# Kernel tuning notes

Measured on AMD Instinct MI355X. Metric: run time of the kernel, lower is better.

The kernel has to match this reference:

```python
import jax, jax.numpy as jnp
import numpy as np

B, S, D = 2, 2048, 2048
H, HD = 16, 128          # num_heads, head_dim (H*HD == D)
I = 4096                 # intermediate_size; ffn in-dim is 2*I
EPS = 1e-5


def rmsnorm(x, w):
    return x * jax.lax.rsqrt(jnp.mean(x * x, axis=-1, keepdims=True) + EPS) * w


def setup_inputs() -> dict:
    key = jax.random.key(0)
    ks = jax.random.split(key, 12)
    sd = 0.02
    return {
        "hidden_states": jax.random.normal(ks[0], (B, S, D), jnp.float32),
        "attention_mask": jnp.zeros((B, S), jnp.float32),  # additive mask
        "rn1_w": jnp.ones((D,), jnp.float32),
        "wq": jax.random.normal(ks[1], (D, D), jnp.float32) * sd,
        "wk": jax.random.normal(ks[2], (D, D), jnp.float32) * sd,
        "wv": jax.random.normal(ks[3], (D, D), jnp.float32) * sd,
        "wo": jax.random.normal(ks[4], (D, D), jnp.float32) * sd,
        "rn2_w": jnp.ones((D,), jnp.float32),
        "w1": jax.random.normal(ks[5], (D, 2 * I), jnp.float32) * sd,      # Linear(d, 2*I, bias=False)
        "fc1_w": jax.random.normal(ks[6], (2 * I, I), jnp.float32) * sd,   # SwiGLU fc1
        "fc1_b": jnp.zeros((I,), jnp.float32),
        "fc2_w": jax.random.normal(ks[7], (2 * I, I), jnp.float32) * sd,   # SwiGLU fc2
        "fc2_b": jnp.zeros((I,), jnp.float32),
        "w3": jax.random.normal(ks[8], (I, D), jnp.float32) * sd,          # Linear(I, d, bias=False)
    }


def reference(hidden_states, attention_mask, rn1_w, wq, wk, wv, wo, rn2_w,
              w1, fc1_w, fc1_b, fc2_w, fc2_b, w3):
    # --- attention ---
    attn_in = rmsnorm(hidden_states, rn1_w)
    q = (attn_in @ wq).reshape(B, S, H, HD)
    k = (attn_in @ wk).reshape(B, S, H, HD)
    v = (attn_in @ wv).reshape(B, S, H, HD)
    # rope_cache is None -> no rotary embedding applied
    scores = jnp.einsum("bqhd,bkhd->bhqk", q, k) / np.sqrt(HD).astype(np.float32)
    scores = scores + attention_mask[:, None, None, :]  # [B,1,1,S] broadcast
    probs = jax.nn.softmax(scores, axis=-1)             # dropout p=0 (eval)
    attn = jnp.einsum("bhqk,bkhd->bqhd", probs, v).reshape(B, S, D)
    residual1 = hidden_states + attn @ wo
    # --- SwiGLU FFN ---
    ffn_in = rmsnorm(residual1, rn2_w)
    x = ffn_in @ w1                                      # [B,S,2I]
    gated = jax.nn.silu(x @ fc1_w + fc1_b) * (x @ fc2_w + fc2_b)  # [B,S,I]
    return residual1 + gated @ w3
```

## Files before the change

### kernel.cpp

```cpp
#include <hip/hip_runtime.h>
#include <hip/hip_bf16.h>
#include <stdint.h>

using short8 = __attribute__((ext_vector_type(8))) short;
using f32x4  = __attribute__((ext_vector_type(4))) float;

#define DEV __device__ __forceinline__

DEV float b2f(unsigned short u) {
  union { unsigned int i; float f; } v; v.i = ((unsigned int)u) << 16; return v.f;
}
DEV unsigned short f2b(float f) {
  union { float f; unsigned int i; } v; v.f = f;
  unsigned int x = v.i;
  return (unsigned short)((x + 0x7FFFu + ((x >> 16) & 1u)) >> 16);
}
DEV void g2lds16(const void* g, void* l) {
  __builtin_amdgcn_global_load_lds((const __attribute__((address_space(1))) void*)g,
                                   (__attribute__((address_space(3))) void*)l, 16, 0, 0);
}

enum { EPI_BF16 = 0, EPI_RESID_F32 = 1, EPI_BIAS_BF16 = 2, EPI_RESID_OUT = 3 };

template<int EPI>
__global__ __launch_bounds__(512, 2)
void gemm_bt256(const unsigned short* __restrict__ A, const unsigned short* __restrict__ Bt,
                void* __restrict__ Cout, const void* __restrict__ extra,
                int M, int N, int K) {
  __shared__ __align__(16) unsigned short As[2][256 * 64];
  __shared__ __align__(16) unsigned short Bs[2][256 * 64];
  const int nbx = N >> 8;
  int wg = blockIdx.x;
  const int nwg = gridDim.x;
  if ((nwg & 7) == 0) wg = (wg & 7) * (nwg >> 3) + (wg >> 3);
  const int by = wg / nbx, bx = wg % nbx;
  const int m0 = by << 8, n0 = bx << 8;
  const int t = threadIdx.x;
  const int l = t & 63, wid = t >> 6;
  const int lr = l & 15, lg = l >> 4;
  const int wr = (wid >> 2) << 7;
  const int wc = (wid & 3) << 6;

  f32x4 acc[8][4];
#pragma unroll
  for (int i = 0; i < 8; ++i)
#pragma unroll
    for (int j = 0; j < 4; ++j) acc[i][j] = (f32x4){0.f, 0.f, 0.f, 0.f};

  const int sr = t >> 3;
  const int scSwz = ((t & 7) << 3) ^ ((sr & 7) << 3);
  const unsigned short* Ag = A  + (size_t)(m0 + sr) * K + scSwz;
  const unsigned short* Bg = Bt + (size_t)(n0 + sr) * K + scSwz;

  const int xorv = (lr & 7) << 3;
  const int cb0 = (lg * 8) ^ xorv;
  const int cb1 = (32 + lg * 8) ^ xorv;

#pragma unroll
  for (int ld = 0; ld < 4; ++ld) {
    g2lds16(Ag + (size_t)(ld * 64) * K, &As[0][0] + t * 8 + ld * 4096);
    g2lds16(Bg + (size_t)(ld * 64) * K, &Bs[0][0] + t * 8 + ld * 4096);
  }
  asm volatile("s_waitcnt vmcnt(0)\n\ts_barrier" ::: "memory");

  int cur = 0;
  for (int kt = 0; kt < K; kt += 64) {
    const unsigned short* Asc = &As[0][0] + cur * 16384;
    const unsigned short* Bsc = &Bs[0][0] + cur * 16384;
    unsigned short* Asn = &As[0][0] + (cur ^ 1) * 16384;
    unsigned short* Bsn = &Bs[0][0] + (cur ^ 1) * 16384;
    const bool has_next = (kt + 64) < K;
    short8 bfr[4][2];
#pragma unroll
    for (int p = 0; p < 4; ++p) {
      short8 af[2][2];
#pragma unroll
      for (int a = 0; a < 2; ++a) {
        const int ro = (wr + (p * 2 + a) * 16 + lr) << 6;
        af[a][0] = *(const short8*)(Asc + ro + cb0);
        af[a][1] = *(const short8*)(Asc + ro + cb1);
      }
      if (p == 0) {
#pragma unroll
        for (int ni = 0; ni < 4; ++ni) {
          const int ro = (wc + ni * 16 + lr) << 6;
          bfr[ni][0] = *(const short8*)(Bsc + ro + cb0);
          bfr[ni][1] = *(const short8*)(Bsc + ro + cb1);
        }
        if (has_next) {
#pragma unroll
          for (int ld = 0; ld < 4; ++ld)
            g2lds16(Ag + (size_t)(ld * 64) * K + (kt + 64), Asn + t * 8 + ld * 4096);
        }
      }
      if (p == 1 && has_next) {
#pragma unroll
        for (int ld = 0; ld < 4; ++ld)
          g2lds16(Bg + (size_t)(ld * 64) * K + (kt + 64), Bsn + t * 8 + ld * 4096);
      }
      asm volatile("s_barrier" ::: "memory");
      asm volatile("s_waitcnt lgkmcnt(0)" ::: "memory");
      __builtin_amdgcn_sched_barrier(0);
      __builtin_amdgcn_s_setprio(1);
#pragma unroll
      for (int kk = 0; kk < 2; ++kk)
#pragma unroll
        for (int a = 0; a < 2; ++a)
#pragma unroll
          for (int ni = 0; ni < 4; ++ni)
            acc[p * 2 + a][ni] =
                __builtin_amdgcn_mfma_f32_16x16x32_bf16(af[a][kk], bfr[ni][kk], acc[p * 2 + a][ni], 0, 0, 0);
      __builtin_amdgcn_s_setprio(0);
      if (p < 3) {
        asm volatile("s_barrier" ::: "memory");
      } else {
        asm volatile("s_waitcnt vmcnt(0)\n\ts_barrier" ::: "memory");
      }
    }
    cur ^= 1;
  }

#pragma unroll
  for (int mi = 0; mi < 8; ++mi) {
#pragma unroll
    for (int ni = 0; ni < 4; ++ni) {
      const int col = n0 + wc + ni * 16 + lr;
#pragma unroll
      for (int j = 0; j < 4; ++j) {
        const int row = m0 + wr + mi * 16 + lg * 4 + j;
        const size_t idx = (size_t)row * N + col;
        const float v = acc[mi][ni][j];
        if constexpr (EPI == EPI_BF16) {
          ((unsigned short*)Cout)[idx] = f2b(v);
        } else if constexpr (EPI == EPI_RESID_F32) {
          ((float*)Cout)[idx] = v + ((const float*)extra)[idx];
        } else if constexpr (EPI == EPI_BIAS_BF16) {
          ((unsigned short*)Cout)[idx] = f2b(v + ((const float*)extra)[col]);
        } else {
          ((float*)Cout)[idx] = v + ((const float*)extra)[idx];
        }
      }
    }
  }
}

template<int EPI>
__global__ __launch_bounds__(256)
void gemm_bt(const unsigned short* __restrict__ A, const unsigned short* __restrict__ Bt,
             void* __restrict__ Cout, const void* __restrict__ extra,
             int M, int N, int K) {
  __shared__ __align__(16) unsigned short As[128 * 64];
  __shared__ __align__(16) unsigned short Bs[128 * 64];
  const int nbx = N >> 7;
  int wg = blockIdx.x;
  const int nwg = gridDim.x;
  if ((nwg & 7) == 0) wg = (wg & 7) * (nwg >> 3) + (wg >> 3);
  const int by = wg / nbx, bx = wg % nbx;
  const int m0 = by << 7, n0 = bx << 7;
  const int t = threadIdx.x;
  const int l = t & 63, w = t >> 6;
  const int lr = l & 15, lg = l >> 4;
  const int wr = (w >> 1) << 6, wc = (w & 1) << 6;

  f32x4 acc[4][4];
#pragma unroll
  for (int i = 0; i < 4; ++i)
#pragma unroll
    for (int j = 0; j < 4; ++j) acc[i][j] = (f32x4){0.f, 0.f, 0.f, 0.f};

  const int sr = t >> 3;
  const int skSwz = ((t & 7) << 3) ^ ((sr & 7) << 3);
  const unsigned short* Ag = A  + (size_t)(m0 + sr) * K + skSwz;
  const unsigned short* Bg = Bt + (size_t)(n0 + sr) * K + skSwz;
  unsigned short* Al = As + t * 8;
  unsigned short* Bl = Bs + t * 8;

  for (int kt = 0; kt < K; kt += 64) {
#pragma unroll
    for (int c = 0; c < 4; ++c) {
      g2lds16(Ag + (size_t)(c * 32) * K + kt, Al + c * 2048);
      g2lds16(Bg + (size_t)(c * 32) * K + kt, Bl + c * 2048);
    }
    __syncthreads();
#pragma unroll
    for (int ks = 0; ks < 2; ++ks) {
      short8 af[4], bfr[4];
#pragma unroll
      for (int mi = 0; mi < 4; ++mi) {
        const int row = wr + mi * 16 + lr;
        af[mi] = *(const short8*)(As + (row << 6) + (((ks * 32 + lg * 8)) ^ ((row & 7) << 3)));
      }
#pragma unroll
      for (int ni = 0; ni < 4; ++ni) {
        const int row = wc + ni * 16 + lr;
        bfr[ni] = *(const short8*)(Bs + (row << 6) + (((ks * 32 + lg * 8)) ^ ((row & 7) << 3)));
      }
#pragma unroll
      for (int mi = 0; mi < 4; ++mi)
#pragma unroll
        for (int ni = 0; ni < 4; ++ni)
          acc[mi][ni] = __builtin_amdgcn_mfma_f32_16x16x32_bf16(af[mi], bfr[ni], acc[mi][ni], 0, 0, 0);
    }
    __syncthreads();
  }

#pragma unroll
  for (int mi = 0; mi < 4; ++mi) {
#pragma unroll
    for (int ni = 0; ni < 4; ++ni) {
      const int col = n0 + wc + ni * 16 + lr;
#pragma unroll
      for (int j = 0; j < 4; ++j) {
        const int row = m0 + wr + mi * 16 + lg * 4 + j;
        const size_t idx = (size_t)row * N + col;
        const float v = acc[mi][ni][j];
        if constexpr (EPI == EPI_BF16) {
          ((unsigned short*)Cout)[idx] = f2b(v);
        } else if constexpr (EPI == EPI_RESID_F32) {
          ((float*)Cout)[idx] = v + ((const float*)extra)[idx];
        } else if constexpr (EPI == EPI_BIAS_BF16) {
          ((unsigned short*)Cout)[idx] = f2b(v + ((const float*)extra)[col]);
        } else {
          ((float*)Cout)[idx] = v + ((const float*)extra)[idx];
        }
      }
    }
  }
}

__global__ __launch_bounds__(256)
void attn_fwd(const unsigned short* __restrict__ qkv, const unsigned short* __restrict__ vt,
              const float* __restrict__ mask, unsigned short* __restrict__ out) {
  __shared__ __align__(16) unsigned short Ks[64 * 128];
  __shared__ __align__(16) unsigned short Vs[128 * 64];
  __shared__ __align__(16) unsigned short Ps[4][16 * 64];
  const int b = blockIdx.z, hh = blockIdx.y;
  const int q0 = blockIdx.x << 6;
  const int t = threadIdx.x, l = t & 63, w = t >> 6;
  const int lr = l & 15, lg = l >> 4;
  const float scale = 0.08838834764831845f;

  short8 qf[4];
  {
    const unsigned short* qb = qkv + (size_t)(b * 2048 + q0 + w * 16 + lr) * 6144 + hh * 128;
#pragma unroll
    for (int ks = 0; ks < 4; ++ks) qf[ks] = *(const short8*)(qb + ks * 32 + lg * 8);
  }
  f32x4 acc_o[8];
#pragma unroll
  for (int i = 0; i < 8; ++i) acc_o[i] = (f32x4){0.f, 0.f, 0.f, 0.f};
  float m_r[4], l_r[4];
#pragma unroll
  for (int j = 0; j < 4; ++j) { m_r[j] = -1e30f; l_r[j] = 0.f; }

  const unsigned short* kb = qkv + (size_t)(b * 2048) * 6144 + 2048 + hh * 128;
  const unsigned short* vb = vt + (size_t)(b * 16 + hh) * 128 * 2048;
  const float* mb = mask + b * 2048;

  for (int kt = 0; kt < 2048; kt += 64) {
#pragma unroll
    for (int c = 0; c < 4; ++c) {
      const int e = (c * 256 + t) * 8;
      const int kr = e >> 7, kc = e & 127;
      g2lds16(kb + (size_t)(kt + kr) * 6144 + (kc ^ ((kr & 7) << 3)), Ks + e);
      const int vr = e >> 6, vc = e & 63;
      g2lds16(vb + (size_t)vr * 2048 + kt + (vc ^ ((vr & 7) << 3)), Vs + e);
    }
    __syncthreads();

    f32x4 sc[4];
#pragma unroll
    for (int nt = 0; nt < 4; ++nt) {
      f32x4 s = (f32x4){0.f, 0.f, 0.f, 0.f};
#pragma unroll
      for (int ks = 0; ks < 4; ++ks) {
        short8 kf = *(const short8*)(Ks + ((nt * 16 + lr) << 7) + ((ks * 32 + lg * 8) ^ ((lr & 7) << 3)));
        s = __builtin_amdgcn_mfma_f32_16x16x32_bf16(qf[ks], kf, s, 0, 0, 0);
      }
      sc[nt] = s;
    }
#pragma unroll
    for (int nt = 0; nt < 4; ++nt) {
      const float mv = mb[kt + nt * 16 + lr];
#pragma unroll
      for (int j = 0; j < 4; ++j) sc[nt][j] = sc[nt][j] * scale + mv;
    }
#pragma unroll
    for (int j = 0; j < 4; ++j) {
      float tm = fmaxf(fmaxf(sc[0][j], sc[1][j]), fmaxf(sc[2][j], sc[3][j]));
      tm = fmaxf(tm, __shfl_xor(tm, 1));
      tm = fmaxf(tm, __shfl_xor(tm, 2));
      tm = fmaxf(tm, __shfl_xor(tm, 4));
      tm = fmaxf(tm, __shfl_xor(tm, 8));
      const float mn = fmaxf(m_r[j], tm);
      const float corr = __expf(m_r[j] - mn);
      m_r[j] = mn;
      float ps = 0.f;
#pragma unroll
      for (int nt = 0; nt < 4; ++nt) {
        const float p = __expf(sc[nt][j] - mn);
        sc[nt][j] = p;
        ps += p;
      }
      ps += __shfl_xor(ps, 1);
      ps += __shfl_xor(ps, 2);
      ps += __shfl_xor(ps, 4);
      ps += __shfl_xor(ps, 8);
      l_r[j] = l_r[j] * corr + ps;
#pragma unroll
      for (int di = 0; di < 8; ++di) acc_o[di][j] *= corr;
    }
#pragma unroll
    for (int nt = 0; nt < 4; ++nt)
#pragma unroll
      for (int j = 0; j < 4; ++j) {
        const int q = lg * 4 + j;
        Ps[w][(q << 6) + ((nt * 16 + lr) ^ ((q & 7) << 3))] = f2b(sc[nt][j]);
      }
    asm volatile("s_waitcnt lgkmcnt(0)" ::: "memory");
#pragma unroll
    for (int ks2 = 0; ks2 < 2; ++ks2) {
      short8 pf = *(const short8*)(&Ps[w][(lr << 6) + ((ks2 * 32 + lg * 8) ^ ((lr & 7) << 3))]);
#pragma unroll
      for (int di = 0; di < 8; ++di) {
        short8 vf = *(const short8*)(Vs + ((di * 16 + lr) << 6) + ((ks2 * 32 + lg * 8) ^ ((lr & 7) << 3)));
        acc_o[di] = __builtin_amdgcn_mfma_f32_16x16x32_bf16(pf, vf, acc_o[di], 0, 0, 0);
      }
    }
    __syncthreads();
  }
#pragma unroll
  for (int di = 0; di < 8; ++di)
#pragma unroll
    for (int j = 0; j < 4; ++j) {
      const int q = q0 + w * 16 + lg * 4 + j;
      out[(size_t)(b * 2048 + q) * 2048 + hh * 128 + di * 16 + lr] = f2b(acc_o[di][j] / l_r[j]);
    }
}

__global__ __launch_bounds__(256)
void rmsnorm_k(const float* __restrict__ in, const float* __restrict__ wgt,
               unsigned short* __restrict__ out) {
  __shared__ float red[4];
  const int row = blockIdx.x, t = threadIdx.x;
  const float4* rp = (const float4*)(in + (size_t)row * 2048 + t * 8);
  float4 a = rp[0], b = rp[1];
  float x[8] = {a.x, a.y, a.z, a.w, b.x, b.y, b.z, b.w};
  float s = 0.f;
#pragma unroll
  for (int i = 0; i < 8; ++i) s += x[i] * x[i];
#pragma unroll
  for (int m = 1; m < 64; m <<= 1) s += __shfl_xor(s, m);
  const int l = t & 63, w = t >> 6;
  if (l == 0) red[w] = s;
  __syncthreads();
  const float tot = red[0] + red[1] + red[2] + red[3];
  const float rr = rsqrtf(tot * (1.f / 2048.f) + 1e-5f);
  const float4* wp = (const float4*)(wgt + t * 8);
  float4 wa = wp[0], wb = wp[1];
  float ww[8] = {wa.x, wa.y, wa.z, wa.w, wb.x, wb.y, wb.z, wb.w};
  short8 o;
#pragma unroll
  for (int i = 0; i < 8; ++i) o[i] = (short)f2b(x[i] * rr * ww[i]);
  *(short8*)(out + (size_t)row * 2048 + t * 8) = o;
}

__global__ __launch_bounds__(256)
void transpose2d(const float* __restrict__ in, unsigned short* __restrict__ out,
                 int R, int C) {
  __shared__ __align__(16) unsigned short tile[64][72];
  const int r0 = blockIdx.y << 6, c0 = blockIdx.x << 6;
  const int t = threadIdx.x;
#pragma unroll
  for (int it = 0; it < 4; ++it) {
    const int e = (it * 256 + t) * 4;
    const int r = e >> 6, cc = e & 63;
    float4 v = *(const float4*)(in + (size_t)(r0 + r) * C + c0 + cc);
    tile[cc + 0][r] = f2b(v.x);
    tile[cc + 1][r] = f2b(v.y);
    tile[cc + 2][r] = f2b(v.z);
    tile[cc + 3][r] = f2b(v.w);
  }
  __syncthreads();
#pragma unroll
  for (int it = 0; it < 2; ++it) {
    const int e = (it * 256 + t) * 8;
    const int rr = e >> 6, kk = e & 63;
    short8 v = *(const short8*)(&tile[rr][kk]);
    *(short8*)(out + (size_t)(c0 + rr) * R + r0 + kk) = v;
  }
}

__global__ __launch_bounds__(256)
void transpose_v(const unsigned short* __restrict__ qkv, unsigned short* __restrict__ vt) {
  __shared__ __align__(16) unsigned short tile[64][72];
  const int s0 = blockIdx.x << 6, d0 = blockIdx.y << 6;
  const int z = blockIdx.z;
  const unsigned short* in = qkv + (size_t)((z >> 4) * 2048) * 6144 + 4096 + (z & 15) * 128;
  unsigned short* outp = vt + (size_t)z * 128 * 2048;
  const int t = threadIdx.x;
#pragma unroll
  for (int it = 0; it < 2; ++it) {
    const int e = (it * 256 + t) * 8;
    const int r = e >> 6, cc = e & 63;
    short8 v = *(const short8*)(in + (size_t)(s0 + r) * 6144 + d0 + cc);
#pragma unroll
    for (int i = 0; i < 8; ++i) tile[cc + i][r] = (unsigned short)v[i];
  }
  __syncthreads();
#pragma unroll
  for (int it = 0; it < 2; ++it) {
    const int e = (it * 256 + t) * 8;
    const int rr = e >> 6, kk = e & 63;
    short8 v = *(const short8*)(&tile[rr][kk]);
    *(short8*)(outp + (size_t)(d0 + rr) * 2048 + s0 + kk) = v;
  }
}

__global__ __launch_bounds__(256)
void swiglu_k(const unsigned short* __restrict__ g1, const unsigned short* __restrict__ g2,
              unsigned short* __restrict__ gated) {
  const size_t i = ((size_t)blockIdx.x * 256 + threadIdx.x) * 8;
  short8 a = *(const short8*)(g1 + i);
  short8 b = *(const short8*)(g2 + i);
  short8 o;
#pragma unroll
  for (int j = 0; j < 8; ++j) {
    const float x = b2f((unsigned short)a[j]);
    const float y = b2f((unsigned short)b[j]);
    o[j] = (short)f2b(x / (1.f + __expf(-x)) * y);
  }
  *(short8*)(gated + i) = o;
}

extern "C" void kernel_launch(void* const* d_in, const int* in_sizes, int n_in,
                              void* d_out, int out_size, void* d_ws, size_t ws_size,
                              hipStream_t stream) {
  const float* h    = (const float*)d_in[0];
  const float* mask = (const float*)d_in[1];
  const float* rn1w = (const float*)d_in[2];
  const float* wq   = (const float*)d_in[3];
  const float* wk   = (const float*)d_in[4];
  const float* wv   = (const float*)d_in[5];
  const float* wo   = (const float*)d_in[6];
  const float* rn2w = (const float*)d_in[7];
  const float* w1   = (const float*)d_in[8];
  const float* fc1w = (const float*)d_in[9];
  const float* fc1b = (const float*)d_in[10];
  const float* fc2w = (const float*)d_in[11];
  const float* fc2b = (const float*)d_in[12];
  const float* w3   = (const float*)d_in[13];

  char* ws = (char*)d_ws;
  size_t off = 0;
  auto alloc = [&](size_t bytes) { char* p = ws + off; off += (bytes + 255) & ~(size_t)255; return p; };
  unsigned short* bufA = (unsigned short*)alloc(16777216);
  unsigned short* bufB = (unsigned short*)alloc(16777216);
  unsigned short* qkv  = (unsigned short*)alloc(50331648);
  float*          r1f  = (float*)alloc(33554432);
  unsigned short* xbuf = (unsigned short*)alloc(67108864);
  unsigned short* g1   = (unsigned short*)alloc(33554432);
  unsigned short* g2   = (unsigned short*)alloc(33554432);
  unsigned short* wt   = (unsigned short*)alloc(67108864);
  if (off > ws_size) return;

  rmsnorm_k<<<4096, 256, 0, stream>>>(h, rn1w, bufA);
  transpose2d<<<dim3(32, 32), 256, 0, stream>>>(wq, wt,                 2048, 2048);
  transpose2d<<<dim3(32, 32), 256, 0, stream>>>(wk, wt + 2048 * 2048,   2048, 2048);
  transpose2d<<<dim3(32, 32), 256, 0, stream>>>(wv, wt + 2 * 2048 * 2048, 2048, 2048);
  gemm_bt256<EPI_BF16><<<384, 512, 0, stream>>>(bufA, wt, qkv, nullptr, 4096, 6144, 2048);
  transpose_v<<<dim3(32, 2, 32), 256, 0, stream>>>(qkv, bufB);
  attn_fwd<<<dim3(32, 16, 2), 256, 0, stream>>>(qkv, bufB, mask, bufA);
  transpose2d<<<dim3(32, 32), 256, 0, stream>>>(wo, wt, 2048, 2048);
  gemm_bt<EPI_RESID_F32><<<512, 256, 0, stream>>>(bufA, wt, r1f, h, 4096, 2048, 2048);

  rmsnorm_k<<<4096, 256, 0, stream>>>(r1f, rn2w, bufB);
  transpose2d<<<dim3(128, 32), 256, 0, stream>>>(w1, wt, 2048, 8192);
  gemm_bt256<EPI_BF16><<<512, 512, 0, stream>>>(bufB, wt, xbuf, nullptr, 4096, 8192, 2048);
  transpose2d<<<dim3(64, 128), 256, 0, stream>>>(fc1w, wt, 8192, 4096);
  gemm_bt256<EPI_BIAS_BF16><<<256, 512, 0, stream>>>(xbuf, wt, g1, fc1b, 4096, 4096, 8192);
  transpose2d<<<dim3(64, 128), 256, 0, stream>>>(fc2w, wt, 8192, 4096);
  gemm_bt256<EPI_BIAS_BF16><<<256, 512, 0, stream>>>(xbuf, wt, g2, fc2b, 4096, 4096, 8192);
  unsigned short* gated = qkv;
  swiglu_k<<<8192, 256, 0, stream>>>(g1, g2, gated);
  transpose2d<<<dim3(32, 64), 256, 0, stream>>>(w3, wt, 4096, 2048);
  gemm_bt<EPI_RESID_OUT><<<512, 256, 0, stream>>>(gated, wt, d_out, r1f, 4096, 2048, 4096);
}
```

Before: 1.225 ms.

## Prefetch B tiles two K-steps ahead using register-held fragments in GEMM pipeline

The GEMM main loop now issues the B-operand global-to-LDS loads two K tiles ahead instead of one, while A stays one tile ahead. This is safe because B fragments for the current tile are already pulled into registers at the first sub-step. Waits are relaxed from vmcnt(0) to vmcnt(4), so the next B tile's loads can stay in flight across the tile boundary. The aim is to hide more global-load latency behind the MFMA work. The cost is that correctness now depends on careful wait-count accounting and barrier ordering.

```diff
diff --git a/kernel.cpp b/kernel.cpp
--- a/kernel.cpp
+++ b/kernel.cpp
@@ -51,25 +51,38 @@
   const int scSwz = ((t & 7) << 3) ^ ((sr & 7) << 3);
   const unsigned short* Ag = A  + (size_t)(m0 + sr) * K + scSwz;
   const unsigned short* Bg = Bt + (size_t)(n0 + sr) * K + scSwz;
+  const int nT = K >> 6;
+
+  auto stageA = [&](int tt, int h) {
+    unsigned short* dst = &As[tt & 1][h * 8192 + t * 8];
+    const unsigned short* src = Ag + (size_t)(h * 128) * K + (tt << 6);
+    g2lds16(src, dst);
+    g2lds16(src + (size_t)64 * K, dst + 4096);
+  };
+  auto stageB = [&](int tt, int h) {
+    unsigned short* dst = &Bs[tt & 1][h * 8192 + t * 8];
+    const unsigned short* src = Bg + (size_t)(h * 128) * K + (tt << 6);
+    g2lds16(src, dst);
+    g2lds16(src + (size_t)64 * K, dst + 4096);
+  };
 
   const int xorv = (lr & 7) << 3;
   const int cb0 = (lg * 8) ^ xorv;
   const int cb1 = (32 + lg * 8) ^ xorv;
 
-#pragma unroll
-  for (int ld = 0; ld < 4; ++ld) {
-    g2lds16(Ag + (size_t)(ld * 64) * K, &As[0][0] + t * 8 + ld * 4096);
-    g2lds16(Bg + (size_t)(ld * 64) * K, &Bs[0][0] + t * 8 + ld * 4096);
-  }
-  asm volatile("s_waitcnt vmcnt(0)\n\ts_barrier" ::: "memory");
-
-  int cur = 0;
-  for (int kt = 0; kt < K; kt += 64) {
-    const unsigned short* Asc = &As[0][0] + cur * 16384;
-    const unsigned short* Bsc = &Bs[0][0] + cur * 16384;
-    unsigned short* Asn = &As[0][0] + (cur ^ 1) * 16384;
-    unsigned short* Bsn = &Bs[0][0] + (cur ^ 1) * 16384;
-    const bool has_next = (kt + 64) < K;
+  stageA(0, 0); stageA(0, 1); stageB(0, 0); stageB(0, 1);
+  if (nT > 1) {
+    stageB(1, 0); stageB(1, 1);
+    asm volatile("s_waitcnt vmcnt(4)" ::: "memory");
+  } else {
+    asm volatile("s_waitcnt vmcnt(0)" ::: "memory");
+  }
+  asm volatile("s_barrier" ::: "memory");
+
+  for (int tt = 0; tt < nT; ++tt) {
+    const int cur = tt & 1;
+    const unsigned short* Asc = &As[cur][0];
+    const unsigned short* Bsc = &Bs[cur][0];
     short8 bfr[4][2];
 #pragma unroll
     for (int p = 0; p < 4; ++p) {
@@ -87,17 +100,11 @@
           bfr[ni][0] = *(const short8*)(Bsc + ro + cb0);
           bfr[ni][1] = *(const short8*)(Bsc + ro + cb1);
         }
-        if (has_next) {
-#pragma unroll
-          for (int ld = 0; ld < 4; ++ld)
-            g2lds16(Ag + (size_t)(ld * 64) * K + (kt + 64), Asn + t * 8 + ld * 4096);
-        }
-      }
-      if (p == 1 && has_next) {
-#pragma unroll
-        for (int ld = 0; ld < 4; ++ld)
-          g2lds16(Bg + (size_t)(ld * 64) * K + (kt + 64), Bsn + t * 8 + ld * 4096);
-      }
+        if (tt + 1 < nT) stageA(tt + 1, 0);
+      }
+      if (p == 1 && tt + 1 < nT) stageA(tt + 1, 1);
+      if (p == 2 && tt + 2 < nT) stageB(tt + 2, 0);
+      if (p == 3 && tt + 2 < nT) stageB(tt + 2, 1);
       asm volatile("s_barrier" ::: "memory");
       asm volatile("s_waitcnt lgkmcnt(0)" ::: "memory");
       __builtin_amdgcn_sched_barrier(0);
@@ -114,10 +121,13 @@
       if (p < 3) {
         asm volatile("s_barrier" ::: "memory");
       } else {
-        asm volatile("s_waitcnt vmcnt(0)\n\ts_barrier" ::: "memory");
-      }
-    }
-    cur ^= 1;
+        if (tt + 1 < nT) {
+          if (tt + 2 < nT) asm volatile("s_waitcnt vmcnt(4)" ::: "memory");
+          else             asm volatile("s_waitcnt vmcnt(0)" ::: "memory");
+        }
+        asm volatile("s_barrier" ::: "memory");
+      }
+    }
   }
 
 #pragma unroll
```

New measurement: 1.267 ms. 1.03x slower.

## Software-pipeline LDS fragment reads with double-buffered A registers in GEMM main loop

Applied to the files above, without the earlier changes.

Restructures the GEMM K-loop so A-fragment LDS reads for the next phase are issued before the MFMAs of the current phase, ping-ponging between two register sets. The next tile's A and B fragments are prefetched at the end of each iteration, and partial lgkmcnt waits replace the full waits. The goal is to hide LDS read latency behind MFMA work and drop some barriers. It uses more VGPRs, which may lower occupancy, and the partial waitcnt counts must match the issued loads exactly.

```diff
diff --git a/kernel.cpp b/kernel.cpp
--- a/kernel.cpp
+++ b/kernel.cpp
@@ -51,74 +51,108 @@
   const int scSwz = ((t & 7) << 3) ^ ((sr & 7) << 3);
   const unsigned short* Ag = A  + (size_t)(m0 + sr) * K + scSwz;
   const unsigned short* Bg = Bt + (size_t)(n0 + sr) * K + scSwz;
+  const int nT = K >> 6;
+
+  auto stageA = [&](int tt) {
+    unsigned short* dst = &As[tt & 1][t * 8];
+    const unsigned short* src = Ag + ((size_t)tt << 6);
+#pragma unroll
+    for (int ld = 0; ld < 4; ++ld) g2lds16(src + (size_t)(ld * 64) * K, dst + ld * 4096);
+  };
+  auto stageB = [&](int tt) {
+    unsigned short* dst = &Bs[tt & 1][t * 8];
+    const unsigned short* src = Bg + ((size_t)tt << 6);
+#pragma unroll
+    for (int ld = 0; ld < 4; ++ld) g2lds16(src + (size_t)(ld * 64) * K, dst + ld * 4096);
+  };
 
   const int xorv = (lr & 7) << 3;
   const int cb0 = (lg * 8) ^ xorv;
   const int cb1 = (32 + lg * 8) ^ xorv;
 
-#pragma unroll
-  for (int ld = 0; ld < 4; ++ld) {
-    g2lds16(Ag + (size_t)(ld * 64) * K, &As[0][0] + t * 8 + ld * 4096);
-    g2lds16(Bg + (size_t)(ld * 64) * K, &Bs[0][0] + t * 8 + ld * 4096);
-  }
+  short8 afA[2][2], afB[2][2], bfr[4][2];
+
+#define READ_A(dst, base, p)                                          \
+  {                                                                   \
+    const int ro0 = (wr + ((p) * 2 + 0) * 16 + lr) << 6;              \
+    const int ro1 = (wr + ((p) * 2 + 1) * 16 + lr) << 6;              \
+    dst[0][0] = *(const short8*)((base) + ro0 + cb0);                 \
+    dst[0][1] = *(const short8*)((base) + ro0 + cb1);                 \
+    dst[1][0] = *(const short8*)((base) + ro1 + cb0);                 \
+    dst[1][1] = *(const short8*)((base) + ro1 + cb1);                 \
+  }
+#define READ_B(base)                                                  \
+  {                                                                   \
+    _Pragma("unroll")                                                 \
+    for (int ni = 0; ni < 4; ++ni) {                                  \
+      const int ro = (wc + ni * 16 + lr) << 6;                        \
+      bfr[ni][0] = *(const short8*)((base) + ro + cb0);               \
+      bfr[ni][1] = *(const short8*)((base) + ro + cb1);               \
+    }                                                                 \
+  }
+#define MFMA_PH(af, r0)                                               \
+  {                                                                   \
+    _Pragma("unroll")                                                 \
+    for (int kk = 0; kk < 2; ++kk)                                    \
+      _Pragma("unroll")                                               \
+      for (int a = 0; a < 2; ++a)                                     \
+        _Pragma("unroll")                                             \
+        for (int ni = 0; ni < 4; ++ni)                                \
+          acc[(r0) + a][ni] = __builtin_amdgcn_mfma_f32_16x16x32_bf16(\
+              af[a][kk], bfr[ni][kk], acc[(r0) + a][ni], 0, 0, 0);    \
+  }
+
+  stageA(0); stageB(0);
   asm volatile("s_waitcnt vmcnt(0)\n\ts_barrier" ::: "memory");
-
-  int cur = 0;
-  for (int kt = 0; kt < K; kt += 64) {
-    const unsigned short* Asc = &As[0][0] + cur * 16384;
-    const unsigned short* Bsc = &Bs[0][0] + cur * 16384;
-    unsigned short* Asn = &As[0][0] + (cur ^ 1) * 16384;
-    unsigned short* Bsn = &Bs[0][0] + (cur ^ 1) * 16384;
-    const bool has_next = (kt + 64) < K;
-    short8 bfr[4][2];
-#pragma unroll
-    for (int p = 0; p < 4; ++p) {
-      short8 af[2][2];
-#pragma unroll
-      for (int a = 0; a < 2; ++a) {
-        const int ro = (wr + (p * 2 + a) * 16 + lr) << 6;
-        af[a][0] = *(const short8*)(Asc + ro + cb0);
-        af[a][1] = *(const short8*)(Asc + ro + cb1);
-      }
-      if (p == 0) {
-#pragma unroll
-        for (int ni = 0; ni < 4; ++ni) {
-          const int ro = (wc + ni * 16 + lr) << 6;
-          bfr[ni][0] = *(const short8*)(Bsc + ro + cb0);
-          bfr[ni][1] = *(const short8*)(Bsc + ro + cb1);
-        }
-        if (has_next) {
-#pragma unroll
-          for (int ld = 0; ld < 4; ++ld)
-            g2lds16(Ag + (size_t)(ld * 64) * K + (kt + 64), Asn + t * 8 + ld * 4096);
-        }
-      }
-      if (p == 1 && has_next) {
-#pragma unroll
-        for (int ld = 0; ld < 4; ++ld)
-          g2lds16(Bg + (size_t)(ld * 64) * K + (kt + 64), Bsn + t * 8 + ld * 4096);
-      }
-      asm volatile("s_barrier" ::: "memory");
-      asm volatile("s_waitcnt lgkmcnt(0)" ::: "memory");
-      __builtin_amdgcn_sched_barrier(0);
-      __builtin_amdgcn_s_setprio(1);
-#pragma unroll
-      for (int kk = 0; kk < 2; ++kk)
-#pragma unroll
-        for (int a = 0; a < 2; ++a)
-#pragma unroll
-          for (int ni = 0; ni < 4; ++ni)
-            acc[p * 2 + a][ni] =
-                __builtin_amdgcn_mfma_f32_16x16x32_bf16(af[a][kk], bfr[ni][kk], acc[p * 2 + a][ni], 0, 0, 0);
-      __builtin_amdgcn_s_setprio(0);
-      if (p < 3) {
-        asm volatile("s_barrier" ::: "memory");
-      } else {
-        asm volatile("s_waitcnt vmcnt(0)\n\ts_barrier" ::: "memory");
-      }
-    }
-    cur ^= 1;
-  }
+  {
+    const unsigned short* base = &As[0][0];
+    const unsigned short* bbase = &Bs[0][0];
+    READ_A(afA, base, 0);
+    READ_B(bbase);
+  }
+
+  for (int tt = 0; tt < nT; ++tt) {
+    const unsigned short* base = &As[tt & 1][0];
+    const bool more = (tt + 1) < nT;
+    READ_A(afB, base, 1);
+    if (more) stageA(tt + 1);
+    asm volatile("s_waitcnt lgkmcnt(4)" ::: "memory");
+    __builtin_amdgcn_sched_barrier(0);
+    __builtin_amdgcn_s_setprio(1);
+    MFMA_PH(afA, 0);
+    __builtin_amdgcn_s_setprio(0);
+    asm volatile("s_barrier" ::: "memory");
+    READ_A(afA, base, 2);
+    if (more) stageB(tt + 1);
+    asm volatile("s_waitcnt lgkmcnt(4)" ::: "memory");
+    __builtin_amdgcn_sched_barrier(0);
+    __builtin_amdgcn_s_setprio(1);
+    MFMA_PH(afB, 2);
+    __builtin_amdgcn_s_setprio(0);
+    asm volatile("s_barrier" ::: "memory");
+    READ_A(afB, base, 3);
+    asm volatile("s_waitcnt lgkmcnt(4)" ::: "memory");
+    __builtin_amdgcn_sched_barrier(0);
+    __builtin_amdgcn_s_setprio(1);
+    MFMA_PH(afA, 4);
+    __builtin_amdgcn_s_setprio(0);
+    asm volatile("s_barrier" ::: "memory");
+    asm volatile("s_waitcnt lgkmcnt(0)" ::: "memory");
+    __builtin_amdgcn_sched_barrier(0);
+    __builtin_amdgcn_s_setprio(1);
+    MFMA_PH(afB, 6);
+    __builtin_amdgcn_s_setprio(0);
+    asm volatile("s_waitcnt vmcnt(0)\n\ts_barrier" ::: "memory");
+    if (more) {
+      const unsigned short* nbase = &As[(tt + 1) & 1][0];
+      const unsigned short* nbbase = &Bs[(tt + 1) & 1][0];
+      READ_A(afA, nbase, 0);
+      READ_B(nbbase);
+    }
+  }
+#undef READ_A
+#undef READ_B
+#undef MFMA_PH
 
 #pragma unroll
   for (int mi = 0; mi < 8; ++mi) {
```

Result: no change. 1.213 ms (-1.0%).
